# Optimization experiments

Hardware: AMD Instinct MI355X
Metric: run time of the kernel (lower is better)

The kernel has to match this reference:

```python
import jax, jax.numpy as jnp
import numpy as np

N = 100000   # nodes
E = 1600000  # edges (avg degree 16)
D = 128      # in_channels == hidden_channels
H = 4        # heads
C = D // H   # per-head channels = 32


def leaky(x, slope):
    return jnp.where(x >= 0, x, slope * x)


def setup_inputs() -> dict:
    key = jax.random.key(0)
    ks = jax.random.split(key, 12)
    s = 1.0 / np.sqrt(D)
    return {
        "x": jax.random.normal(ks[0], (N, D), jnp.float32),
        "edge_index": jax.random.randint(ks[1], (2, E), 0, N, jnp.int32),
        "edge_type": jax.random.randint(ks[2], (E,), 0, 8, jnp.int32),
        # linear1 (first_layer=True): LeakyReLU(0.01) -> Linear(D, D)
        "W1": jax.random.normal(ks[3], (D, D), jnp.float32) * s,
        "b1": jnp.zeros((D,), jnp.float32),
        # GATConv params: lin (no bias), att_src/att_dst [1,H,C], output bias [H*C]
        "Wg": jax.random.normal(ks[4], (D, D), jnp.float32) * s,
        "att_src": jax.random.normal(ks[5], (1, H, C), jnp.float32) * s,
        "att_dst": jax.random.normal(ks[6], (1, H, C), jnp.float32) * s,
        "bias_g": jnp.zeros((D,), jnp.float32),
        # linear2: LeakyReLU(0.01) -> Linear(D, D)
        "W2": jax.random.normal(ks[7], (D, D), jnp.float32) * s,
        "b2": jnp.zeros((D,), jnp.float32),
    }


def reference(x, edge_index, edge_type, W1, b1, Wg, att_src, att_dst, bias_g, W2, b2):
    # dropout layers act in eval mode (identity); edge_type is unused by forward.
    # linear1: LeakyReLU(0.01) then Linear
    x = leaky(x, 0.01) @ W1.T + b1                      # [N, D]

    # GATConv (add_self_loops=False, concat heads)
    h = (x @ Wg.T).reshape(N, H, C)                     # [N, H, C]
    a_src = jnp.sum(h * att_src, axis=-1)               # [N, H]
    a_dst = jnp.sum(h * att_dst, axis=-1)               # [N, H]

    src, dst = edge_index[0], edge_index[1]
    alpha = leaky(a_src[src] + a_dst[dst], 0.2)          # [E, H]

    # segment softmax over destination nodes (numerically stable)
    amax = jax.ops.segment_max(alpha, dst, num_segments=N)   # [N, H], -inf for empty
    amax = jnp.where(jnp.isfinite(amax), amax, 0.0)
    ex = jnp.exp(alpha - amax[dst])                      # [E, H]
    denom = jax.ops.segment_sum(ex, dst, num_segments=N) # [N, H]
    coeff = ex / (denom[dst] + 1e-16)                    # [E, H]

    msg = h[src] * coeff[:, :, None]                     # [E, H, C]
    out = jax.ops.segment_sum(msg, dst, num_segments=N)  # [N, H, C]
    out = out.reshape(N, H * C) + bias_g                 # [N, D]

    # linear2: LeakyReLU(0.01) then Linear; Dropout(0.3) identity at eval
    out = leaky(out, 0.01) @ W2.T + b2                   # [N, D]
    return out
```

## Files before the change

kernel.cpp:

```cpp
#include <hip/hip_runtime.h>
#include <hip/hip_bf16.h>

#define D128 128

typedef __attribute__((ext_vector_type(8))) short bf16x8;
typedef __attribute__((ext_vector_type(4))) float f32x4;

__device__ __forceinline__ float b2f(unsigned short u) {
    union { unsigned int i; float f; } z;
    z.i = ((unsigned int)u) << 16;
    return z.f;
}

__device__ __forceinline__ unsigned short f2b(float f) {
    union { float f; unsigned int i; } z;
    z.f = f;
    unsigned int r = z.i + 0x7FFFu + ((z.i >> 16) & 1u);
    return (unsigned short)(r >> 16);
}

__device__ __forceinline__ f32x4 mfma16(bf16x8 a, bf16x8 b, f32x4 c) {
    return __builtin_amdgcn_mfma_f32_16x16x32_bf16(a, b, c, 0, 0, 0);
}

#define XBB 1536

__global__ __launch_bounds__(256) void k_prep1(
    const float* __restrict__ x,
    const float* __restrict__ W1, const float* __restrict__ Wg,
    const float* __restrict__ b1,
    float* __restrict__ Wc, float* __restrict__ bc,
    unsigned short* __restrict__ xb, int N)
{
    __shared__ float wgr[256];
    const int t = threadIdx.x;
    if (blockIdx.x < 64) {
        const int i0 = blockIdx.x * 2;
        wgr[t] = Wg[i0 * 128 + t];
        __syncthreads();
        const int half = t >> 7;
        const int j = t & 127;
        const float* wr = &wgr[half * 128];
        float acc = 0.f;
        #pragma unroll 4
        for (int k = 0; k < 128; ++k)
            acc += wr[k] * W1[k * 128 + j];
        Wc[(i0 + half) * 128 + j] = acc;
        if (j == 0) {
            float ab = 0.f;
            for (int k = 0; k < 128; ++k) ab += wr[k] * b1[k];
            bc[i0 + half] = ab;
        }
    } else {
        const size_t total = (size_t)N * 128;
        const size_t stride = (size_t)XBB * 256 * 8;
        for (size_t i = ((size_t)(blockIdx.x - 64) * 256 + t) * 8; i + 8 <= total; i += stride) {
            float4 f0 = *(const float4*)(x + i);
            float4 f1 = *(const float4*)(x + i + 4);
            float v[8] = { f0.x, f0.y, f0.z, f0.w, f1.x, f1.y, f1.z, f1.w };
            union { uint4 q; unsigned short s[8]; } o;
            #pragma unroll
            for (int jj = 0; jj < 8; ++jj) {
                float f = v[jj];
                f = f >= 0.f ? f : 0.01f * f;
                o.s[jj] = f2b(f);
            }
            *(uint4*)(xb + i) = o.q;
        }
    }
}

__global__ __launch_bounds__(256) void k_prep2(
    const float* __restrict__ Wc, const float* __restrict__ bc,
    const float* __restrict__ att_s, const float* __restrict__ att_d,
    const float* __restrict__ W2,
    unsigned short* __restrict__ Wcat, unsigned short* __restrict__ W2l,
    float* __restrict__ lbias)
{
    const int b = blockIdx.x, t = threadIdx.x;
    if (b < 9) {
        const int q = b * 256 + t;
        const int ct = q >> 8, rem = q & 255;
        const int ks = rem >> 6, lane = rem & 63;
        const int ldiv = lane >> 4, lmod = lane & 15;
        const int kb = ks * 32 + ldiv * 8;
        float v[8];
        if (ct < 8) {
            const int rho = ct * 16 + lmod;
            const float4 a = *(const float4*)(Wc + rho * 128 + kb);
            const float4 bq = *(const float4*)(Wc + rho * 128 + kb + 4);
            v[0] = a.x; v[1] = a.y; v[2] = a.z; v[3] = a.w;
            v[4] = bq.x; v[5] = bq.y; v[6] = bq.z; v[7] = bq.w;
        } else {
            #pragma unroll
            for (int e = 0; e < 8; ++e) v[e] = 0.f;
            if (lmod < 8) {
                const int hh = lmod & 3;
                const float* av = lmod < 4 ? att_s : att_d;
                for (int c = 0; c < 32; ++c) {
                    const float w = av[hh * 32 + c];
                    const float* wrow = Wc + (hh * 32 + c) * 128 + kb;
                    #pragma unroll
                    for (int e = 0; e < 8; ++e) v[e] += w * wrow[e];
                }
            }
        }
        union { uint4 qq; unsigned short s[8]; } o;
        #pragma unroll
        for (int e = 0; e < 8; ++e) o.s[e] = f2b(v[e]);
        *(uint4*)(Wcat + q * 8) = o.qq;
    } else if (b < 17) {
        const int q = (b - 9) * 256 + t;
        const int ct = q >> 8, rem = q & 255;
        const int ks = rem >> 6, lane = rem & 63;
        const int ldiv = lane >> 4, lmod = lane & 15;
        const int kb = ks * 32 + ldiv * 8;
        const int rho = ct * 16 + lmod;
        const float4 a = *(const float4*)(W2 + rho * 128 + kb);
        const float4 bq = *(const float4*)(W2 + rho * 128 + kb + 4);
        union { uint4 qq; unsigned short s[8]; } o;
        o.s[0] = f2b(a.x); o.s[1] = f2b(a.y); o.s[2] = f2b(a.z); o.s[3] = f2b(a.w);
        o.s[4] = f2b(bq.x); o.s[5] = f2b(bq.y); o.s[6] = f2b(bq.z); o.s[7] = f2b(bq.w);
        *(uint4*)(W2l + q * 8) = o.qq;
    } else {
        if (t < 144) {
            float v = 0.f;
            if (t < 128) v = bc[t];
            else if (t < 136) {
                const int hh = (t - 128) & 3;
                const float* av = t < 132 ? att_s : att_d;
                for (int c = 0; c < 32; ++c) v += av[hh * 32 + c] * bc[hh * 32 + c];
            }
            lbias[t] = v;
        }
    }
}

__global__ __launch_bounds__(256) void k_gemm_h(
    const unsigned short* __restrict__ xb,
    const unsigned short* __restrict__ Wcat,
    const float* __restrict__ lbias,
    unsigned short* __restrict__ hfeat,
    float* __restrict__ asrc, float* __restrict__ adst, int N)
{
    __shared__ __align__(16) unsigned short sW[18432];
    const int t = threadIdx.x;
    const int wave = t >> 6, lane = t & 63, lmod = lane & 15, ldiv = lane >> 4;
    const int rowBase = blockIdx.x * 64;

    uint4 w[9];
    #pragma unroll
    for (int r = 0; r < 9; ++r)
        w[r] = *(const uint4*)(Wcat + r * 2048 + t * 8);

    int row = rowBase + wave * 16 + lmod;
    row = min(row, N - 1);
    bf16x8 afr[4];
    #pragma unroll
    for (int ks = 0; ks < 4; ++ks)
        afr[ks] = *(const bf16x8*)(xb + (size_t)row * D128 + ks * 32 + ldiv * 8);

    #pragma unroll
    for (int r = 0; r < 9; ++r)
        *(uint4*)&sW[r * 2048 + t * 8] = w[r];
    __syncthreads();

    f32x4 acc[9] = {};
    #pragma unroll
    for (int ct = 0; ct < 9; ++ct) {
        #pragma unroll
        for (int ks = 0; ks < 4; ++ks) {
            bf16x8 bfr = *(const bf16x8*)&sW[(ct * 256 + ks * 64 + lane) * 8];
            acc[ct] = mfma16(afr[ks], bfr, acc[ct]);
        }
    }

    const int orow = rowBase + wave * 16 + ldiv * 4;
    #pragma unroll
    for (int ct = 0; ct < 8; ++ct) {
        const int col = ct * 16 + lmod;
        const float bias = lbias[col];
        #pragma unroll
        for (int r = 0; r < 4; ++r)
            if (orow + r < N)
                hfeat[(size_t)(orow + r) * D128 + col] = f2b(acc[ct][r] + bias);
    }
    if (lmod < 8) {
        const float lb = lbias[128 + lmod];
        float* dst = lmod < 4 ? asrc : adst;
        const int hh = lmod & 3;
        #pragma unroll
        for (int r = 0; r < 4; ++r)
            if (orow + r < N)
                dst[(size_t)(orow + r) * 4 + hh] = acc[8][r] + lb;
    }
}

#define CHUNK 8192
#define MAXBINS 512
#define BINCAP 8192

__global__ __launch_bounds__(256) void kA1(
    const int* __restrict__ ei, int* __restrict__ M,
    int E, int B, int nbins)
{
    __shared__ int hist[MAXBINS];
    for (int i = threadIdx.x; i < nbins; i += 256) hist[i] = 0;
    __syncthreads();
    const int base = blockIdx.x * CHUNK;
    const int end = min(base + CHUNK, E);
    for (int e = base + threadIdx.x; e < end; e += 256)
        atomicAdd(&hist[ei[E + e] >> 8], 1);
    __syncthreads();
    for (int i = threadIdx.x; i < nbins; i += 256)
        M[i * B + blockIdx.x] = hist[i];
}

__global__ __launch_bounds__(1024) void k_scan1(
    const int* __restrict__ in, int* __restrict__ scanned,
    int* __restrict__ bsum, int n)
{
    __shared__ int lds[1024];
    const int gid = blockIdx.x * 1024 + threadIdx.x;
    const int v = gid < n ? in[gid] : 0;
    lds[threadIdx.x] = v;
    __syncthreads();
    #pragma unroll
    for (int off = 1; off < 1024; off <<= 1) {
        int t = threadIdx.x >= off ? lds[threadIdx.x - off] : 0;
        __syncthreads();
        lds[threadIdx.x] += t;
        __syncthreads();
    }
    if (gid < n) scanned[gid] = lds[threadIdx.x] - v;
    if (threadIdx.x == 1023) bsum[blockIdx.x] = lds[1023];
}

__global__ __launch_bounds__(1024) void k_scan2(int* __restrict__ bsum, int nb)
{
    __shared__ int lds[1024];
    const int v = threadIdx.x < nb ? bsum[threadIdx.x] : 0;
    lds[threadIdx.x] = v;
    __syncthreads();
    #pragma unroll
    for (int off = 1; off < 1024; off <<= 1) {
        int t = threadIdx.x >= off ? lds[threadIdx.x - off] : 0;
        __syncthreads();
        lds[threadIdx.x] += t;
        __syncthreads();
    }
    if (threadIdx.x < nb) bsum[threadIdx.x] = lds[threadIdx.x] - v;
}

__global__ __launch_bounds__(256) void kA2(
    const int* __restrict__ ei, const int* __restrict__ scanned,
    const int* __restrict__ bsum, int2* __restrict__ binned,
    int E, int B, int nbins)
{
    __shared__ int cursor[MAXBINS];
    for (int i = threadIdx.x; i < nbins; i += 256) {
        const int idx = i * B + blockIdx.x;
        cursor[i] = scanned[idx] + bsum[idx >> 10];
    }
    __syncthreads();
    const int base = blockIdx.x * CHUNK;
    const int end = min(base + CHUNK, E);
    for (int e = base + threadIdx.x; e < end; e += 256) {
        const int s = ei[e], d = ei[E + e];
        const int pos = atomicAdd(&cursor[d >> 8], 1);
        binned[pos] = make_int2(s, d);
    }
}

__global__ __launch_bounds__(256) void kB(
    const int2* __restrict__ binned, const int* __restrict__ scanned,
    const int* __restrict__ bsum, int* __restrict__ bucket,
    int* __restrict__ rowstart, int* __restrict__ rowend,
    int E, int B, int nbins, int N)
{
    __shared__ int2 eb[BINCAP];
    __shared__ int ldeg[256];
    __shared__ int lscan[256];
    __shared__ int lcur[256];
    const int bin = blockIdx.x;
    const int i0 = bin * B;
    const int binstart = scanned[i0] + bsum[i0 >> 10];
    int binend;
    if (bin + 1 < nbins) {
        const int i1 = (bin + 1) * B;
        binend = scanned[i1] + bsum[i1 >> 10];
    } else {
        binend = E;
    }
    int n = binend - binstart;
    if (n > BINCAP) n = BINCAP;

    for (int i = threadIdx.x; i < n; i += 256) eb[i] = binned[binstart + i];
    ldeg[threadIdx.x] = 0;
    __syncthreads();
    for (int i = threadIdx.x; i < n; i += 256)
        atomicAdd(&ldeg[eb[i].y & 255], 1);
    __syncthreads();
    const int v = ldeg[threadIdx.x];
    lscan[threadIdx.x] = v;
    __syncthreads();
    #pragma unroll
    for (int off = 1; off < 256; off <<= 1) {
        int t = threadIdx.x >= off ? lscan[threadIdx.x - off] : 0;
        __syncthreads();
        lscan[threadIdx.x] += t;
        __syncthreads();
    }
    const int excl = lscan[threadIdx.x] - v;
    lcur[threadIdx.x] = excl;
    const int d = (bin << 8) + threadIdx.x;
    if (d < N) {
        rowstart[d] = binstart + excl;
        rowend[d]   = binstart + excl + v;
    }
    __syncthreads();
    for (int i = threadIdx.x; i < n; i += 256) {
        const int lp = atomicAdd(&lcur[eb[i].y & 255], 1);
        bucket[binstart + lp] = eb[i].x;
    }
}

__global__ __launch_bounds__(256) void k_gat(
    const int* __restrict__ bucket,
    const int* __restrict__ rowstart, const int* __restrict__ rowend,
    const float* __restrict__ asrc, const float* __restrict__ adst,
    const unsigned short* __restrict__ hfeat,
    const float* __restrict__ bias_g,
    unsigned short* __restrict__ outbf, int N)
{
    const int wave = threadIdx.x >> 6;
    const int lane = threadIdx.x & 63;
    const int g    = lane >> 4;
    const int gl   = lane & 15;
    const int h    = gl >> 2;
    const int d    = blockIdx.x * 16 + wave * 4 + g;

    int start = 0, end = 0;
    float a_d = 0.f;
    if (d < N) {
        start = rowstart[d];
        end   = rowend[d];
        a_d   = adst[(size_t)d * 4 + h];
    }
    const unsigned int chb = (unsigned int)(gl << 3);

    float acc[8] = {0.f, 0.f, 0.f, 0.f, 0.f, 0.f, 0.f, 0.f};
    float denom = 0.f;

    int j = start;
    for (; j + 2 <= end; j += 2) {
        const int s0 = bucket[j];
        const int s1 = bucket[j + 1];
        const float as0 = asrc[((size_t)s0 << 2) + h];
        const float as1 = asrc[((size_t)s1 << 2) + h];
        const uint4 hp0 = *(const uint4*)(hfeat + (((unsigned int)s0 << 7) + chb));
        const uint4 hp1 = *(const uint4*)(hfeat + (((unsigned int)s1 << 7) + chb));
        float a0 = as0 + a_d; a0 = a0 >= 0.f ? a0 : 0.2f * a0;
        float a1 = as1 + a_d; a1 = a1 >= 0.f ? a1 : 0.2f * a1;
        const float w0 = __expf(a0), w1 = __expf(a1);
        denom += w0 + w1;
        const unsigned int u00 = hp0.x, u01 = hp0.y, u02 = hp0.z, u03 = hp0.w;
        const unsigned int u10 = hp1.x, u11 = hp1.y, u12 = hp1.z, u13 = hp1.w;
        acc[0] += w0 * b2f((unsigned short)(u00 & 0xFFFFu)) + w1 * b2f((unsigned short)(u10 & 0xFFFFu));
        acc[1] += w0 * b2f((unsigned short)(u00 >> 16))     + w1 * b2f((unsigned short)(u10 >> 16));
        acc[2] += w0 * b2f((unsigned short)(u01 & 0xFFFFu)) + w1 * b2f((unsigned short)(u11 & 0xFFFFu));
        acc[3] += w0 * b2f((unsigned short)(u01 >> 16))     + w1 * b2f((unsigned short)(u11 >> 16));
        acc[4] += w0 * b2f((unsigned short)(u02 & 0xFFFFu)) + w1 * b2f((unsigned short)(u12 & 0xFFFFu));
        acc[5] += w0 * b2f((unsigned short)(u02 >> 16))     + w1 * b2f((unsigned short)(u12 >> 16));
        acc[6] += w0 * b2f((unsigned short)(u03 & 0xFFFFu)) + w1 * b2f((unsigned short)(u13 & 0xFFFFu));
        acc[7] += w0 * b2f((unsigned short)(u03 >> 16))     + w1 * b2f((unsigned short)(u13 >> 16));
    }
    if (j < end) {
        const int s0 = bucket[j];
        const float as0 = asrc[((size_t)s0 << 2) + h];
        const uint4 hp0 = *(const uint4*)(hfeat + (((unsigned int)s0 << 7) + chb));
        float a0 = as0 + a_d; a0 = a0 >= 0.f ? a0 : 0.2f * a0;
        const float w0 = __expf(a0);
        denom += w0;
        acc[0] += w0 * b2f((unsigned short)(hp0.x & 0xFFFFu));
        acc[1] += w0 * b2f((unsigned short)(hp0.x >> 16));
        acc[2] += w0 * b2f((unsigned short)(hp0.y & 0xFFFFu));
        acc[3] += w0 * b2f((unsigned short)(hp0.y >> 16));
        acc[4] += w0 * b2f((unsigned short)(hp0.z & 0xFFFFu));
        acc[5] += w0 * b2f((unsigned short)(hp0.z >> 16));
        acc[6] += w0 * b2f((unsigned short)(hp0.w & 0xFFFFu));
        acc[7] += w0 * b2f((unsigned short)(hp0.w >> 16));
    }

    if (d < N) {
        const float inv = 1.f / (denom + 1e-16f);
        const float4 bg0 = *(const float4*)(bias_g + chb);
        const float4 bg1 = *(const float4*)(bias_g + chb + 4);
        const float bg[8] = { bg0.x, bg0.y, bg0.z, bg0.w, bg1.x, bg1.y, bg1.z, bg1.w };
        unsigned short s[8];
        #pragma unroll
        for (int k2 = 0; k2 < 8; ++k2) {
            float v = acc[k2] * inv + bg[k2];
            v = v >= 0.f ? v : 0.01f * v;
            s[k2] = f2b(v);
        }
        uint4 o;
        o.x = ((unsigned int)s[1] << 16) | s[0];
        o.y = ((unsigned int)s[3] << 16) | s[2];
        o.z = ((unsigned int)s[5] << 16) | s[4];
        o.w = ((unsigned int)s[7] << 16) | s[6];
        *(uint4*)(outbf + (((unsigned int)d << 7) + chb)) = o;
    }
}

__global__ __launch_bounds__(256) void k_final(
    const unsigned short* __restrict__ gatbf,
    const unsigned short* __restrict__ W2l,
    const float* __restrict__ b2,
    float* __restrict__ out, int N)
{
    __shared__ __align__(16) unsigned short sW[16384];
    const int t = threadIdx.x;
    const int wave = t >> 6, lane = t & 63, lmod = lane & 15, ldiv = lane >> 4;
    const int rowBase = blockIdx.x * 64;

    uint4 w[8];
    #pragma unroll
    for (int r = 0; r < 8; ++r)
        w[r] = *(const uint4*)(W2l + r * 2048 + t * 8);

    int row = rowBase + wave * 16 + lmod;
    row = min(row, N - 1);
    bf16x8 afr[4];
    #pragma unroll
    for (int ks = 0; ks < 4; ++ks)
        afr[ks] = *(const bf16x8*)(gatbf + (size_t)row * D128 + ks * 32 + ldiv * 8);

    #pragma unroll
    for (int r = 0; r < 8; ++r)
        *(uint4*)&sW[r * 2048 + t * 8] = w[r];
    __syncthreads();

    f32x4 acc[8] = {};
    #pragma unroll
    for (int ct = 0; ct < 8; ++ct) {
        #pragma unroll
        for (int ks = 0; ks < 4; ++ks) {
            bf16x8 bfr = *(const bf16x8*)&sW[(ct * 256 + ks * 64 + lane) * 8];
            acc[ct] = mfma16(afr[ks], bfr, acc[ct]);
        }
    }

    const int orow = rowBase + wave * 16 + ldiv * 4;
    #pragma unroll
    for (int ct = 0; ct < 8; ++ct) {
        const int col = ct * 16 + lmod;
        const float bb = b2[col];
        #pragma unroll
        for (int r = 0; r < 4; ++r)
            if (orow + r < N)
                out[(size_t)(orow + r) * D128 + col] = acc[ct][r] + bb;
    }
}

extern "C" void kernel_launch(void* const* d_in, const int* in_sizes, int n_in,
                              void* d_out, int out_size, void* d_ws, size_t ws_size,
                              hipStream_t stream)
{
    const float* x    = (const float*)d_in[0];
    const int*   ei   = (const int*)d_in[1];
    const float* W1   = (const float*)d_in[3];
    const float* b1   = (const float*)d_in[4];
    const float* Wg   = (const float*)d_in[5];
    const float* atts = (const float*)d_in[6];
    const float* attd = (const float*)d_in[7];
    const float* bg   = (const float*)d_in[8];
    const float* W2   = (const float*)d_in[9];
    const float* b2   = (const float*)d_in[10];
    float* out = (float*)d_out;

    const int N = in_sizes[0] / D128;
    const int E = in_sizes[1] / 2;

    const int B     = (E + CHUNK - 1) / CHUNK;
    const int nbins = (N + 255) >> 8;
    const int nM    = nbins * B;

    char* ws = (char*)d_ws;
    float* Wc = (float*)ws;
    size_t off = 65536;
    float* bc    = (float*)(ws + off); off += 512;
    float* lbias = (float*)(ws + off); off += 1024;
    unsigned short* Wcat = (unsigned short*)(ws + off); off += 36864;
    unsigned short* W2l  = (unsigned short*)(ws + off); off += 32768;
    unsigned short* xb   = (unsigned short*)(ws + off); off += (size_t)N * D128 * 2;
    unsigned short* hfeat = (unsigned short*)(ws + off); off += (size_t)N * D128 * 2;
    float* asrc = (float*)(ws + off); off += (size_t)N * 4 * 4;
    float* adst = (float*)(ws + off); off += (size_t)N * 4 * 4;
    int* M       = (int*)(ws + off); off += (size_t)nM * 4;
    int* scanned = (int*)(ws + off); off += (size_t)nM * 4;
    int* bsum    = (int*)(ws + off); off += 1024 * 4;
    int2* binned = (int2*)(ws + off); off += (size_t)E * 8;
    int* bucket  = (int*)(ws + off); off += (size_t)E * 4;
    int* rowstart = (int*)(ws + off); off += (size_t)N * 4;
    int* rowend   = (int*)(ws + off); off += (size_t)N * 4;
    unsigned short* outbf = (unsigned short*)(ws + off); off += (size_t)N * D128 * 2;

    k_prep1<<<64 + XBB, 256, 0, stream>>>(x, W1, Wg, b1, Wc, bc, xb, N);
    k_prep2<<<18, 256, 0, stream>>>(Wc, bc, atts, attd, W2, Wcat, W2l, lbias);

    const int nbg = (N + 63) / 64;
    k_gemm_h<<<nbg, 256, 0, stream>>>(xb, Wcat, lbias, hfeat, asrc, adst, N);

    kA1<<<B, 256, 0, stream>>>(ei, M, E, B, nbins);
    const int nsb = (nM + 1023) / 1024;
    k_scan1<<<nsb, 1024, 0, stream>>>(M, scanned, bsum, nM);
    k_scan2<<<1, 1024, 0, stream>>>(bsum, nsb);
    kA2<<<B, 256, 0, stream>>>(ei, scanned, bsum, binned, E, B, nbins);
    kB<<<nbins, 256, 0, stream>>>(binned, scanned, bsum, bucket,
                                  rowstart, rowend, E, B, nbins, N);

    k_gat<<<(N + 15) / 16, 256, 0, stream>>>(bucket, rowstart, rowend,
                                             asrc, adst, hfeat, bg, outbf, N);

    k_final<<<nbg, 256, 0, stream>>>(outbf, W2l, b2, out, N);
}
```

Baseline: 315.5 us.

## Fold histogram into prep kernel, inline block-sum scan, unroll GAT gather by four

The destination-bin histogram kernel is merged into k_prep1 as an extra set of blocks, and the single-block k_scan2 is dropped; kA2 and kB each redo the small serial prefix over block sums in shared memory. Together these remove two kernel launches and their serialization gaps. The GAT aggregation loop now processes four edges per iteration instead of two, with a scalar remainder loop, to put more gather loads in flight. The trade-off is redundant serial scan work in every kA2/kB block and higher register pressure in k_gat.

```diff
diff --git a/kernel.cpp b/kernel.cpp
--- a/kernel.cpp
+++ b/kernel.cpp
@@ -23,16 +23,22 @@
     return __builtin_amdgcn_mfma_f32_16x16x32_bf16(a, b, c, 0, 0, 0);
 }
 
+#define CHUNK 8192
+#define MAXBINS 512
+#define BINCAP 8192
 #define XBB 1536
 
 __global__ __launch_bounds__(256) void k_prep1(
     const float* __restrict__ x,
     const float* __restrict__ W1, const float* __restrict__ Wg,
     const float* __restrict__ b1,
+    const int* __restrict__ ei, int* __restrict__ M,
     float* __restrict__ Wc, float* __restrict__ bc,
-    unsigned short* __restrict__ xb, int N)
+    unsigned short* __restrict__ xb,
+    int N, int E, int B, int nbins)
 {
     __shared__ float wgr[256];
+    __shared__ int hist[MAXBINS];
     const int t = threadIdx.x;
     if (blockIdx.x < 64) {
         const int i0 = blockIdx.x * 2;
@@ -51,10 +57,21 @@
             for (int k = 0; k < 128; ++k) ab += wr[k] * b1[k];
             bc[i0 + half] = ab;
         }
+    } else if (blockIdx.x < 64 + B) {
+        const int chunk = blockIdx.x - 64;
+        for (int i = t; i < nbins; i += 256) hist[i] = 0;
+        __syncthreads();
+        const int base = chunk * CHUNK;
+        const int end = min(base + CHUNK, E);
+        for (int e = base + t; e < end; e += 256)
+            atomicAdd(&hist[ei[E + e] >> 8], 1);
+        __syncthreads();
+        for (int i = t; i < nbins; i += 256)
+            M[i * B + chunk] = hist[i];
     } else {
         const size_t total = (size_t)N * 128;
         const size_t stride = (size_t)XBB * 256 * 8;
-        for (size_t i = ((size_t)(blockIdx.x - 64) * 256 + t) * 8; i + 8 <= total; i += stride) {
+        for (size_t i = ((size_t)(blockIdx.x - 64 - B) * 256 + t) * 8; i + 8 <= total; i += stride) {
             float4 f0 = *(const float4*)(x + i);
             float4 f1 = *(const float4*)(x + i + 4);
             float v[8] = { f0.x, f0.y, f0.z, f0.w, f1.x, f1.y, f1.z, f1.w };
@@ -196,26 +213,6 @@
     }
 }
 
-#define CHUNK 8192
-#define MAXBINS 512
-#define BINCAP 8192
-
-__global__ __launch_bounds__(256) void kA1(
-    const int* __restrict__ ei, int* __restrict__ M,
-    int E, int B, int nbins)
-{
-    __shared__ int hist[MAXBINS];
-    for (int i = threadIdx.x; i < nbins; i += 256) hist[i] = 0;
-    __syncthreads();
-    const int base = blockIdx.x * CHUNK;
-    const int end = min(base + CHUNK, E);
-    for (int e = base + threadIdx.x; e < end; e += 256)
-        atomicAdd(&hist[ei[E + e] >> 8], 1);
-    __syncthreads();
-    for (int i = threadIdx.x; i < nbins; i += 256)
-        M[i * B + blockIdx.x] = hist[i];
-}
-
 __global__ __launch_bounds__(1024) void k_scan1(
     const int* __restrict__ in, int* __restrict__ scanned,
     int* __restrict__ bsum, int n)
@@ -236,31 +233,24 @@
     if (threadIdx.x == 1023) bsum[blockIdx.x] = lds[1023];
 }
 
-__global__ __launch_bounds__(1024) void k_scan2(int* __restrict__ bsum, int nb)
-{
-    __shared__ int lds[1024];
-    const int v = threadIdx.x < nb ? bsum[threadIdx.x] : 0;
-    lds[threadIdx.x] = v;
-    __syncthreads();
-    #pragma unroll
-    for (int off = 1; off < 1024; off <<= 1) {
-        int t = threadIdx.x >= off ? lds[threadIdx.x - off] : 0;
-        __syncthreads();
-        lds[threadIdx.x] += t;
-        __syncthreads();
-    }
-    if (threadIdx.x < nb) bsum[threadIdx.x] = lds[threadIdx.x] - v;
-}
-
 __global__ __launch_bounds__(256) void kA2(
     const int* __restrict__ ei, const int* __restrict__ scanned,
     const int* __restrict__ bsum, int2* __restrict__ binned,
-    int E, int B, int nbins)
+    int E, int B, int nbins, int nM)
 {
     __shared__ int cursor[MAXBINS];
+    __shared__ int bpre[1024];
+    const int nsb = (nM + 1023) >> 10;
+    for (int i = threadIdx.x; i < nsb; i += 256) bpre[i] = bsum[i];
+    __syncthreads();
+    if (threadIdx.x == 0) {
+        int run = 0;
+        for (int i = 0; i < nsb; ++i) { int tv = bpre[i]; bpre[i] = run; run += tv; }
+    }
+    __syncthreads();
     for (int i = threadIdx.x; i < nbins; i += 256) {
         const int idx = i * B + blockIdx.x;
-        cursor[i] = scanned[idx] + bsum[idx >> 10];
+        cursor[i] = scanned[idx] + bpre[idx >> 10];
     }
     __syncthreads();
     const int base = blockIdx.x * CHUNK;
@@ -276,19 +266,28 @@
     const int2* __restrict__ binned, const int* __restrict__ scanned,
     const int* __restrict__ bsum, int* __restrict__ bucket,
     int* __restrict__ rowstart, int* __restrict__ rowend,
-    int E, int B, int nbins, int N)
+    int E, int B, int nbins, int N, int nM)
 {
     __shared__ int2 eb[BINCAP];
     __shared__ int ldeg[256];
     __shared__ int lscan[256];
     __shared__ int lcur[256];
+    __shared__ int bpre[1024];
+    const int nsb = (nM + 1023) >> 10;
+    for (int i = threadIdx.x; i < nsb; i += 256) bpre[i] = bsum[i];
+    __syncthreads();
+    if (threadIdx.x == 0) {
+        int run = 0;
+        for (int i = 0; i < nsb; ++i) { int tv = bpre[i]; bpre[i] = run; run += tv; }
+    }
+    __syncthreads();
     const int bin = blockIdx.x;
     const int i0 = bin * B;
-    const int binstart = scanned[i0] + bsum[i0 >> 10];
+    const int binstart = scanned[i0] + bpre[i0 >> 10];
     int binend;
     if (bin + 1 < nbins) {
         const int i1 = (bin + 1) * B;
-        binend = scanned[i1] + bsum[i1 >> 10];
+        binend = scanned[i1] + bpre[i1 >> 10];
     } else {
         binend = E;
     }
@@ -348,37 +347,53 @@
         a_d   = adst[(size_t)d * 4 + h];
     }
     const unsigned int chb = (unsigned int)(gl << 3);
+    const unsigned short* hbase = hfeat + chb;
 
     float acc[8] = {0.f, 0.f, 0.f, 0.f, 0.f, 0.f, 0.f, 0.f};
     float denom = 0.f;
 
     int j = start;
-    for (; j + 2 <= end; j += 2) {
+    for (; j + 4 <= end; j += 4) {
         const int s0 = bucket[j];
         const int s1 = bucket[j + 1];
+        const int s2 = bucket[j + 2];
+        const int s3 = bucket[j + 3];
         const float as0 = asrc[((size_t)s0 << 2) + h];
         const float as1 = asrc[((size_t)s1 << 2) + h];
-        const uint4 hp0 = *(const uint4*)(hfeat + (((unsigned int)s0 << 7) + chb));
-        const uint4 hp1 = *(const uint4*)(hfeat + (((unsigned int)s1 << 7) + chb));
+        const float as2 = asrc[((size_t)s2 << 2) + h];
+        const float as3 = asrc[((size_t)s3 << 2) + h];
+        const uint4 hp0 = *(const uint4*)(hbase + ((unsigned int)s0 << 7));
+        const uint4 hp1 = *(const uint4*)(hbase + ((unsigned int)s1 << 7));
+        const uint4 hp2 = *(const uint4*)(hbase + ((unsigned int)s2 << 7));
+        const uint4 hp3 = *(const uint4*)(hbase + ((unsigned int)s3 << 7));
         float a0 = as0 + a_d; a0 = a0 >= 0.f ? a0 : 0.2f * a0;
         float a1 = as1 + a_d; a1 = a1 >= 0.f ? a1 : 0.2f * a1;
+        float a2 = as2 + a_d; a2 = a2 >= 0.f ? a2 : 0.2f * a2;
+        float a3 = as3 + a_d; a3 = a3 >= 0.f ? a3 : 0.2f * a3;
         const float w0 = __expf(a0), w1 = __expf(a1);
-        denom += w0 + w1;
-        const unsigned int u00 = hp0.x, u01 = hp0.y, u02 = hp0.z, u03 = hp0.w;
-        const unsigned int u10 = hp1.x, u11 = hp1.y, u12 = hp1.z, u13 = hp1.w;
-        acc[0] += w0 * b2f((unsigned short)(u00 & 0xFFFFu)) + w1 * b2f((unsigned short)(u10 & 0xFFFFu));
-        acc[1] += w0 * b2f((unsigned short)(u00 >> 16))     + w1 * b2f((unsigned short)(u10 >> 16));
-        acc[2] += w0 * b2f((unsigned short)(u01 & 0xFFFFu)) + w1 * b2f((unsigned short)(u11 & 0xFFFFu));
-        acc[3] += w0 * b2f((unsigned short)(u01 >> 16))     + w1 * b2f((unsigned short)(u11 >> 16));
-        acc[4] += w0 * b2f((unsigned short)(u02 & 0xFFFFu)) + w1 * b2f((unsigned short)(u12 & 0xFFFFu));
-        acc[5] += w0 * b2f((unsigned short)(u02 >> 16))     + w1 * b2f((unsigned short)(u12 >> 16));
-        acc[6] += w0 * b2f((unsigned short)(u03 & 0xFFFFu)) + w1 * b2f((unsigned short)(u13 & 0xFFFFu));
-        acc[7] += w0 * b2f((unsigned short)(u03 >> 16))     + w1 * b2f((unsigned short)(u13 >> 16));
-    }
-    if (j < end) {
+        const float w2 = __expf(a2), w3 = __expf(a3);
+        denom += (w0 + w1) + (w2 + w3);
+        acc[0] += w0 * b2f((unsigned short)(hp0.x & 0xFFFFu)) + w1 * b2f((unsigned short)(hp1.x & 0xFFFFu))
+                + w2 * b2f((unsigned short)(hp2.x & 0xFFFFu)) + w3 * b2f((unsigned short)(hp3.x & 0xFFFFu));
+        acc[1] += w0 * b2f((unsigned short)(hp0.x >> 16))     + w1 * b2f((unsigned short)(hp1.x >> 16))
+                + w2 * b2f((unsigned short)(hp2.x >> 16))     + w3 * b2f((unsigned short)(hp3.x >> 16));
+        acc[2] += w0 * b2f((unsigned short)(hp0.y & 0xFFFFu)) + w1 * b2f((unsigned short)(hp1.y & 0xFFFFu))
+                + w2 * b2f((unsigned short)(hp2.y & 0xFFFFu)) + w3 * b2f((unsigned short)(hp3.y & 0xFFFFu));
+        acc[3] += w0 * b2f((unsigned short)(hp0.y >> 16))     + w1 * b2f((unsigned short)(hp1.y >> 16))
+                + w2 * b2f((unsigned short)(hp2.y >> 16))     + w3 * b2f((unsigned short)(hp3.y >> 16));
+        acc[4] += w0 * b2f((unsigned short)(hp0.z & 0xFFFFu)) + w1 * b2f((unsigned short)(hp1.z & 0xFFFFu))
+                + w2 * b2f((unsigned short)(hp2.z & 0xFFFFu)) + w3 * b2f((unsigned short)(hp3.z & 0xFFFFu));
+        acc[5] += w0 * b2f((unsigned short)(hp0.z >> 16))     + w1 * b2f((unsigned short)(hp1.z >> 16))
+                + w2 * b2f((unsigned short)(hp2.z >> 16))     + w3 * b2f((unsigned short)(hp3.z >> 16));
+        acc[6] += w0 * b2f((unsigned short)(hp0.w & 0xFFFFu)) + w1 * b2f((unsigned short)(hp1.w & 0xFFFFu))
+                + w2 * b2f((unsigned short)(hp2.w & 0xFFFFu)) + w3 * b2f((unsigned short)(hp3.w & 0xFFFFu));
+        acc[7] += w0 * b2f((unsigned short)(hp0.w >> 16))     + w1 * b2f((unsigned short)(hp1.w >> 16))
+                + w2 * b2f((unsigned short)(hp2.w >> 16))     + w3 * b2f((unsigned short)(hp3.w >> 16));
+    }
+    for (; j < end; ++j) {
         const int s0 = bucket[j];
         const float as0 = asrc[((size_t)s0 << 2) + h];
-        const uint4 hp0 = *(const uint4*)(hfeat + (((unsigned int)s0 << 7) + chb));
+        const uint4 hp0 = *(const uint4*)(hbase + ((unsigned int)s0 << 7));
         float a0 = as0 + a_d; a0 = a0 >= 0.f ? a0 : 0.2f * a0;
         const float w0 = __expf(a0);
         denom += w0;
@@ -506,19 +521,18 @@
     int* rowend   = (int*)(ws + off); off += (size_t)N * 4;
     unsigned short* outbf = (unsigned short*)(ws + off); off += (size_t)N * D128 * 2;
 
-    k_prep1<<<64 + XBB, 256, 0, stream>>>(x, W1, Wg, b1, Wc, bc, xb, N);
+    k_prep1<<<64 + B + XBB, 256, 0, stream>>>(x, W1, Wg, b1, ei, M, Wc, bc, xb,
+                                              N, E, B, nbins);
     k_prep2<<<18, 256, 0, stream>>>(Wc, bc, atts, attd, W2, Wcat, W2l, lbias);
 
     const int nbg = (N + 63) / 64;
     k_gemm_h<<<nbg, 256, 0, stream>>>(xb, Wcat, lbias, hfeat, asrc, adst, N);
 
-    kA1<<<B, 256, 0, stream>>>(ei, M, E, B, nbins);
     const int nsb = (nM + 1023) / 1024;
     k_scan1<<<nsb, 1024, 0, stream>>>(M, scanned, bsum, nM);
-    k_scan2<<<1, 1024, 0, stream>>>(bsum, nsb);
-    kA2<<<B, 256, 0, stream>>>(ei, scanned, bsum, binned, E, B, nbins);
+    kA2<<<B, 256, 0, stream>>>(ei, scanned, bsum, binned, E, B, nbins, nM);
     kB<<<nbins, 256, 0, stream>>>(binned, scanned, bsum, bucket,
-                                  rowstart, rowend, E, B, nbins, N);
+                                  rowstart, rowend, E, B, nbins, N, nM);
 
     k_gat<<<(N + 15) / 16, 256, 0, stream>>>(bucket, rowstart, rowend,
                                              asrc, adst, hfeat, bg, outbf, N);
```

After: 302.6 us. 1.04x faster.
